# Kernel tuning notes

Measured on AMD Instinct MI355X. Metric: run time of the kernel, lower is better.

## Reference

```python
import jax, jax.numpy as jnp
import numpy as np

MARGIN = 50.0

def setup_inputs() -> dict:
    key = jax.random.key(0)
    k1, k2 = jax.random.split(key)
    N, D = 4096, 768
    rep_anchor = jax.random.normal(k1, (N, D), dtype=jnp.float32)
    rep_pos = jax.random.normal(k2, (N, D), dtype=jnp.float32)
    return {"rep_anchor": rep_anchor, "rep_pos": rep_pos}

def reference(rep_anchor, rep_pos):
    # pairwise euclidean distances: dist[i, j] = ||anchor_i - pos_j||_2
    # (F.pairwise_distance with p=2, eps handled implicitly; use stable sqrt)
    a2 = jnp.sum(rep_anchor * rep_anchor, axis=1, keepdims=True)   # [N,1]
    p2 = jnp.sum(rep_pos * rep_pos, axis=1, keepdims=True).T       # [1,N]
    cross = rep_anchor @ rep_pos.T                                  # [N,N]
    sq = jnp.maximum(a2 + p2 - 2.0 * cross, 0.0)
    dist = jnp.sqrt(sq + 1e-12)
    scores = MARGIN - dist                                          # [N,N]
    # row-wise negative log-softmax, take diagonal (positive pair at index i)
    logp = jax.nn.log_softmax(scores, axis=1)
    loss_per_row = -jnp.diagonal(logp)                               # [N]
    return loss_per_row.mean()
```

## Files before the change

kernel.cpp:

```cpp
#include <hip/hip_runtime.h>
#include <hip/hip_bf16.h>
#include <hip/hip_fp8.h>
#include <stdint.h>


#define N_ROWS 4096
#define D_DIM  768
#define GRID_DIM (N_ROWS / 128)
#define NITER (D_DIM / 128)

typedef float f32x4 __attribute__((ext_vector_type(4)));
typedef int   i32x4 __attribute__((ext_vector_type(4)));

__global__ __launch_bounds__(256) void cvt_norms(
        const float* __restrict__ A, const float* __restrict__ P,
        uint8_t* __restrict__ A8, uint8_t* __restrict__ P8,
        float* __restrict__ a2, float* __restrict__ p2, float* __restrict__ S) {
    const int t = threadIdx.x, lane = t & 63, wave = t >> 6;
    const int row = blockIdx.x * 4 + wave;
    const float* src = blockIdx.y ? P : A;
    uint8_t* dst = blockIdx.y ? P8 : A8;
    float* nrm = blockIdx.y ? p2 : a2;

    const float4* s4 = (const float4*)src + (size_t)row * (D_DIM / 4);
    uint32_t* d4 = (uint32_t*)dst + (size_t)row * (D_DIM / 4);
    float s = 0.0f;
#pragma unroll
    for (int c = 0; c < 3; c++) {
        const int wf = c * 64 + lane;
        float4 v = s4[wf];
        s += v.x * v.x + v.y * v.y + v.z * v.z + v.w * v.w;
        union { uint32_t u; uint8_t b[4]; } pk;
        pk.b[0] = __hip_fp8_e4m3(v.x).__x;
        pk.b[1] = __hip_fp8_e4m3(v.y).__x;
        pk.b[2] = __hip_fp8_e4m3(v.z).__x;
        pk.b[3] = __hip_fp8_e4m3(v.w).__x;
        const int w = wf & 31;
        const int wp = (((w >> 1) & 3) << 3) | ((w >> 3) << 1) | (w & 1);
        d4[(wf & ~31) | wp] = pk.u;
    }
    for (int off = 32; off; off >>= 1) s += __shfl_down(s, off);
    if (lane == 0) {
        nrm[row] = s;
        if (blockIdx.y == 0) S[row] = 0.0f;
    }
}

__device__ __forceinline__ void g2l16(const void* g, void* l) {
    __builtin_amdgcn_global_load_lds(
        (const __attribute__((address_space(1))) void*)g,
        (__attribute__((address_space(3))) void*)l, 16, 0, 0);
}

__global__ __launch_bounds__(256) void gemm_fused(
        const uint8_t* __restrict__ A8, const uint8_t* __restrict__ P8,
        const float* __restrict__ a2, const float* __restrict__ p2,
        float* __restrict__ S, float* __restrict__ Dd) {
    __shared__ __align__(16) uint8_t As[2][128 * 128];
    __shared__ __align__(16) uint8_t Bs[2][128 * 128];

    const int bm = blockIdx.x, bn = blockIdx.y;
    const int t = threadIdx.x;
    const int lane = t & 63, wave = t >> 6;
    const int wm = wave >> 1, wn = wave & 1;

    f32x4 acc[4][4];
#pragma unroll
    for (int i = 0; i < 4; i++)
#pragma unroll
        for (int j = 0; j < 4; j++) acc[i][j] = (f32x4){0.f, 0.f, 0.f, 0.f};

    const int rT = t >> 3;
    const int sg = (t & 7) ^ (rT & 7);
    const size_t aBase = (size_t)(bm * 128 + rT) * D_DIM + (size_t)sg * 16;
    const size_t bBase = (size_t)(bn * 128 + rT) * D_DIM + (size_t)sg * 16;

    const int fr = lane & 15, fq = lane >> 4;
    const int xr = fr & 7;
    const int aRow = (wm * 64 + fr) * 128;
    const int bRow = (wn * 64 + fr) * 128;
    const int cA0 = (((fq << 1) | 0) ^ xr) * 16;
    const int cA1 = (((fq << 1) | 1) ^ xr) * 16;

#define STAGE(K2, SEL)                                                             \
    do {                                                                           \
        const int k0_ = (K2) * 128;                                                \
        _Pragma("unroll")                                                          \
        for (int c = 0; c < 4; c++)                                                \
            g2l16(A8 + aBase + c * (32 * D_DIM) + k0_, &As[SEL][(c * 256 + t) * 16]); \
        _Pragma("unroll")                                                          \
        for (int c = 0; c < 4; c++)                                                \
            g2l16(P8 + bBase + c * (32 * D_DIM) + k0_, &Bs[SEL][(c * 256 + t) * 16]); \
    } while (0)

    STAGE(0, 0);

    for (int k = 0; k < NITER; k++) {
        const int cur = k & 1;
        asm volatile("s_waitcnt vmcnt(0)" ::: "memory");
        asm volatile("s_barrier" ::: "memory");
        if (k + 1 < NITER) STAGE(k + 1, cur ^ 1);

#pragma unroll
        for (int h = 0; h < 2; h++) {
            const int co = h ? cA1 : cA0;
            i32x4 av[4], bv[4];
#pragma unroll
            for (int mi = 0; mi < 4; mi++)
                av[mi] = *(const i32x4*)&As[cur][aRow + mi * (16 * 128) + co];
#pragma unroll
            for (int ni = 0; ni < 4; ni++)
                bv[ni] = *(const i32x4*)&Bs[cur][bRow + ni * (16 * 128) + co];
#pragma unroll
            for (int half = 0; half < 2; half++) {
#pragma unroll
                for (int mi = 0; mi < 4; mi++) {
                    const long long afh = ((const long long*)&av[mi])[half];
#pragma unroll
                    for (int ni = 0; ni < 4; ni++) {
                        const long long bfh = ((const long long*)&bv[ni])[half];
                        acc[mi][ni] = __builtin_amdgcn_mfma_f32_16x16x32_fp8_fp8(
                            afh, bfh, acc[mi][ni], 0, 0, 0);
                    }
                }
            }
        }
    }
#undef STAGE

    float p2v[4];
#pragma unroll
    for (int ni = 0; ni < 4; ni++)
        p2v[ni] = p2[bn * 128 + wn * 64 + ni * 16 + fr];
    const int colBase = bn * 128 + wn * 64 + fr;

#pragma unroll
    for (int mi = 0; mi < 4; mi++) {
#pragma unroll
        for (int r = 0; r < 4; r++) {
            const int gi = bm * 128 + wm * 64 + mi * 16 + fq * 4 + r;
            const float a2v = a2[gi];
            float rs = 0.0f;
#pragma unroll
            for (int ni = 0; ni < 4; ni++) {
                const float cross = acc[mi][ni][r];
                const float sq = a2v + p2v[ni] - 2.0f * cross;
                const float dist = sqrtf(fmaxf(sq, 0.0f) + 1e-12f);
                const int gj = colBase + ni * 16;
                if (gi == gj) Dd[gi] = dist;
                rs += __expf(-dist);
            }
            rs += __shfl_xor(rs, 1);
            rs += __shfl_xor(rs, 2);
            rs += __shfl_xor(rs, 4);
            rs += __shfl_xor(rs, 8);
            if (fr == 0) atomicAdd(&S[gi], rs);
        }
    }
}

__global__ void finalize(const float* __restrict__ S, const float* __restrict__ Dd,
                         float* __restrict__ out) {
    const int t = threadIdx.x;
    float s = 0.0f;
    for (int i = t; i < N_ROWS; i += 256) s += Dd[i] + logf(S[i]);
    for (int off = 32; off; off >>= 1) s += __shfl_down(s, off);
    __shared__ float wsum[4];
    if ((t & 63) == 0) wsum[t >> 6] = s;
    __syncthreads();
    if (t == 0) out[0] = (wsum[0] + wsum[1] + wsum[2] + wsum[3]) * (1.0f / N_ROWS);
}

__global__ void zero_out1(float* __restrict__ out) {
    if (threadIdx.x == 0 && blockIdx.x == 0) out[0] = 0.0f;
}
__global__ void naive_row(const float* __restrict__ A, const float* __restrict__ P,
                          float* __restrict__ out) {
    __shared__ float arow[D_DIM];
    const int i = blockIdx.x, t = threadIdx.x;
    for (int c = t; c < D_DIM; c += 256) arow[c] = A[(size_t)i * D_DIM + c];
    __syncthreads();
    float sumexp = 0.0f, ddiag = 0.0f;
    for (int j = t; j < N_ROWS; j += 256) {
        const float* p = P + (size_t)j * D_DIM;
        float d2 = 0.0f;
        for (int c = 0; c < D_DIM; c++) { float df = arow[c] - p[c]; d2 += df * df; }
        float dist = sqrtf(fmaxf(d2, 0.0f) + 1e-12f);
        if (j == i) ddiag = dist;
        sumexp += __expf(-dist);
    }
    for (int off = 32; off; off >>= 1) {
        sumexp += __shfl_down(sumexp, off);
        ddiag  += __shfl_down(ddiag, off);
    }
    __shared__ float w1[4], w2[4];
    if ((t & 63) == 0) { w1[t >> 6] = sumexp; w2[t >> 6] = ddiag; }
    __syncthreads();
    if (t == 0) {
        float se = w1[0] + w1[1] + w1[2] + w1[3];
        float dd = w2[0] + w2[1] + w2[2] + w2[3];
        atomicAdd(out, (dd + logf(se)) * (1.0f / N_ROWS));
    }
}

extern "C" void kernel_launch(void* const* d_in, const int* in_sizes, int n_in,
                              void* d_out, int out_size, void* d_ws, size_t ws_size,
                              hipStream_t stream) {
    const float* A = (const float*)d_in[0];
    const float* P = (const float*)d_in[1];
    float* out = (float*)d_out;

    const size_t F8_BYTES = (size_t)N_ROWS * D_DIM;
    const size_t V_BYTES  = (size_t)N_ROWS * sizeof(float);
    const size_t NEED = 2 * F8_BYTES + 4 * V_BYTES;

    if (ws_size >= NEED) {
        char* ws = (char*)d_ws;
        uint8_t* A8 = (uint8_t*)(ws);
        uint8_t* P8 = (uint8_t*)(ws + F8_BYTES);
        float* a2 = (float*)(ws + 2 * F8_BYTES);
        float* p2 = (float*)(ws + 2 * F8_BYTES + V_BYTES);
        float* S  = (float*)(ws + 2 * F8_BYTES + 2 * V_BYTES);
        float* Dd = (float*)(ws + 2 * F8_BYTES + 3 * V_BYTES);

        hipLaunchKernelGGL(cvt_norms, dim3(N_ROWS / 4, 2), dim3(256), 0, stream,
                           A, P, A8, P8, a2, p2, S);
        hipLaunchKernelGGL(gemm_fused, dim3(GRID_DIM, GRID_DIM), dim3(256), 0, stream,
                           A8, P8, a2, p2, S, Dd);
        hipLaunchKernelGGL(finalize, dim3(1), dim3(256), 0, stream, S, Dd, out);
    } else {
        hipLaunchKernelGGL(zero_out1, dim3(1), dim3(64), 0, stream, out);
        hipLaunchKernelGGL(naive_row, dim3(N_ROWS), dim3(256), 0, stream, A, P, out);
    }
}
```

Before: 115.1 us.

## Enlarge GEMM tile to 256x128 with K-step 64 and new LDS swizzle

The fused FP8 distance GEMM moves from 128x128 tiles with a K-step of 128 to 256x128 tiles with a K-step of 64. Each wave now computes a 128x64 sub-tile, and the grid is flattened to 1D. The FP8 conversion kernel writes data in a new interleaved order that matches a rotated LDS swizzle for 64-byte rows. The larger tile raises reuse of the B operand and MFMA density per LDS load, but it doubles accumulator registers, which may lower occupancy, and halves the block count to 512.

```diff
diff --git a/kernel.cpp b/kernel.cpp
--- a/kernel.cpp
+++ b/kernel.cpp
@@ -6,8 +6,7 @@
 
 #define N_ROWS 4096
 #define D_DIM  768
-#define GRID_DIM (N_ROWS / 128)
-#define NITER (D_DIM / 128)
+#define NITER (D_DIM / 64)
 
 typedef float f32x4 __attribute__((ext_vector_type(4)));
 typedef int   i32x4 __attribute__((ext_vector_type(4)));
@@ -35,9 +34,10 @@
         pk.b[1] = __hip_fp8_e4m3(v.y).__x;
         pk.b[2] = __hip_fp8_e4m3(v.z).__x;
         pk.b[3] = __hip_fp8_e4m3(v.w).__x;
-        const int w = wf & 31;
-        const int wp = (((w >> 1) & 3) << 3) | ((w >> 3) << 1) | (w & 1);
-        d4[(wf & ~31) | wp] = pk.u;
+        const int kb = wf >> 4, w16 = wf & 15;
+        const int gw = w16 >> 1, h = w16 & 1;
+        const int gp = ((gw & 3) << 1) | (gw >> 2);
+        d4[(kb << 4) + (gp << 1) + h] = pk.u;
     }
     for (int off = 32; off; off >>= 1) s += __shfl_down(s, off);
     if (lane == 0) {
@@ -56,41 +56,50 @@
         const uint8_t* __restrict__ A8, const uint8_t* __restrict__ P8,
         const float* __restrict__ a2, const float* __restrict__ p2,
         float* __restrict__ S, float* __restrict__ Dd) {
-    __shared__ __align__(16) uint8_t As[2][128 * 128];
-    __shared__ __align__(16) uint8_t Bs[2][128 * 128];
-
-    const int bm = blockIdx.x, bn = blockIdx.y;
+    __shared__ __align__(16) uint8_t As[2][256 * 64];
+    __shared__ __align__(16) uint8_t Bs[2][128 * 64];
+
+    const int bid = blockIdx.x;
+    const int bm = bid >> 5, bn = bid & 31;
+
     const int t = threadIdx.x;
     const int lane = t & 63, wave = t >> 6;
     const int wm = wave >> 1, wn = wave & 1;
 
-    f32x4 acc[4][4];
-#pragma unroll
-    for (int i = 0; i < 4; i++)
+    f32x4 acc[8][4];
+#pragma unroll
+    for (int i = 0; i < 8; i++)
 #pragma unroll
         for (int j = 0; j < 4; j++) acc[i][j] = (f32x4){0.f, 0.f, 0.f, 0.f};
 
-    const int rT = t >> 3;
-    const int sg = (t & 7) ^ (rT & 7);
-    const size_t aBase = (size_t)(bm * 128 + rT) * D_DIM + (size_t)sg * 16;
-    const size_t bBase = (size_t)(bn * 128 + rT) * D_DIM + (size_t)sg * 16;
+    const int gT = ((t & 3) - (t >> 3)) & 3;
+    const size_t aBase = (size_t)(bm * 256 + (t >> 2)) * D_DIM + (size_t)gT * 16;
+    const size_t bBase = (size_t)(bn * 128 + (t >> 2)) * D_DIM + (size_t)gT * 16;
 
     const int fr = lane & 15, fq = lane >> 4;
-    const int xr = fr & 7;
-    const int aRow = (wm * 64 + fr) * 128;
-    const int bRow = (wn * 64 + fr) * 128;
-    const int cA0 = (((fq << 1) | 0) ^ xr) * 16;
-    const int cA1 = (((fq << 1) | 1) ^ xr) * 16;
-
-#define STAGE(K2, SEL)                                                             \
-    do {                                                                           \
-        const int k0_ = (K2) * 128;                                                \
-        _Pragma("unroll")                                                          \
-        for (int c = 0; c < 4; c++)                                                \
-            g2l16(A8 + aBase + c * (32 * D_DIM) + k0_, &As[SEL][(c * 256 + t) * 16]); \
-        _Pragma("unroll")                                                          \
-        for (int c = 0; c < 4; c++)                                                \
-            g2l16(P8 + bBase + c * (32 * D_DIM) + k0_, &Bs[SEL][(c * 256 + t) * 16]); \
+    int aOff[8], bOff[4];
+#pragma unroll
+    for (int mi = 0; mi < 8; mi++) {
+        const int R = wm * 128 + mi * 16 + fr;
+        aOff[mi] = R * 64 + ((fq + (R >> 1)) & 3) * 16;
+    }
+#pragma unroll
+    for (int ni = 0; ni < 4; ni++) {
+        const int R = wn * 64 + ni * 16 + fr;
+        bOff[ni] = R * 64 + ((fq + (R >> 1)) & 3) * 16;
+    }
+
+#define STAGE(K2, SEL)                                                            \
+    do {                                                                          \
+        const int k0_ = (K2) * 64;                                                \
+        _Pragma("unroll")                                                         \
+        for (int c = 0; c < 4; c++)                                               \
+            g2l16(A8 + aBase + (size_t)c * (64 * D_DIM) + k0_,                    \
+                  &As[SEL][(c * 256 + t) * 16]);                                  \
+        _Pragma("unroll")                                                         \
+        for (int c = 0; c < 2; c++)                                               \
+            g2l16(P8 + bBase + (size_t)c * (64 * D_DIM) + k0_,                    \
+                  &Bs[SEL][(c * 256 + t) * 16]);                                  \
     } while (0)
 
     STAGE(0, 0);
@@ -101,27 +110,23 @@
         asm volatile("s_barrier" ::: "memory");
         if (k + 1 < NITER) STAGE(k + 1, cur ^ 1);
 
-#pragma unroll
-        for (int h = 0; h < 2; h++) {
-            const int co = h ? cA1 : cA0;
-            i32x4 av[4], bv[4];
-#pragma unroll
-            for (int mi = 0; mi < 4; mi++)
-                av[mi] = *(const i32x4*)&As[cur][aRow + mi * (16 * 128) + co];
-#pragma unroll
-            for (int ni = 0; ni < 4; ni++)
-                bv[ni] = *(const i32x4*)&Bs[cur][bRow + ni * (16 * 128) + co];
-#pragma unroll
-            for (int half = 0; half < 2; half++) {
-#pragma unroll
-                for (int mi = 0; mi < 4; mi++) {
-                    const long long afh = ((const long long*)&av[mi])[half];
-#pragma unroll
-                    for (int ni = 0; ni < 4; ni++) {
-                        const long long bfh = ((const long long*)&bv[ni])[half];
-                        acc[mi][ni] = __builtin_amdgcn_mfma_f32_16x16x32_fp8_fp8(
-                            afh, bfh, acc[mi][ni], 0, 0, 0);
-                    }
+        i32x4 av[8], bv[4];
+#pragma unroll
+        for (int mi = 0; mi < 8; mi++)
+            av[mi] = *(const i32x4*)&As[cur][aOff[mi]];
+#pragma unroll
+        for (int ni = 0; ni < 4; ni++)
+            bv[ni] = *(const i32x4*)&Bs[cur][bOff[ni]];
+#pragma unroll
+        for (int step = 0; step < 2; step++) {
+#pragma unroll
+            for (int mi = 0; mi < 8; mi++) {
+                const long long afh = ((const long long*)&av[mi])[step];
+#pragma unroll
+                for (int ni = 0; ni < 4; ni++) {
+                    const long long bfh = ((const long long*)&bv[ni])[step];
+                    acc[mi][ni] = __builtin_amdgcn_mfma_f32_16x16x32_fp8_fp8(
+                        afh, bfh, acc[mi][ni], 0, 0, 0);
                 }
             }
         }
@@ -135,10 +140,10 @@
     const int colBase = bn * 128 + wn * 64 + fr;
 
 #pragma unroll
-    for (int mi = 0; mi < 4; mi++) {
+    for (int mi = 0; mi < 8; mi++) {
 #pragma unroll
         for (int r = 0; r < 4; r++) {
-            const int gi = bm * 128 + wm * 64 + mi * 16 + fq * 4 + r;
+            const int gi = bm * 256 + wm * 128 + mi * 16 + fq * 4 + r;
             const float a2v = a2[gi];
             float rs = 0.0f;
 #pragma unroll
@@ -225,8 +230,8 @@
 
         hipLaunchKernelGGL(cvt_norms, dim3(N_ROWS / 4, 2), dim3(256), 0, stream,
                            A, P, A8, P8, a2, p2, S);
-        hipLaunchKernelGGL(gemm_fused, dim3(GRID_DIM, GRID_DIM), dim3(256), 0, stream,
-                           A8, P8, a2, p2, S, Dd);
+        hipLaunchKernelGGL(gemm_fused, dim3((N_ROWS / 256) * (N_ROWS / 128)), dim3(256),
+                           0, stream, A8, P8, a2, p2, S, Dd);
         hipLaunchKernelGGL(finalize, dim3(1), dim3(256), 0, stream, S, Dd, out);
     } else {
         hipLaunchKernelGGL(zero_out1, dim3(1), dim3(64), 0, stream, out);
```

New measurement: 155.8 us. +35.3%, slower.
